# Kernel optimization log

Hardware: AMD Instinct MI355X
Metric: run time of the kernel (lower is better)

The kernel has to match this reference:

```python
import jax, jax.numpy as jnp
import numpy as np
import math

D_MODEL = 512
EXPAND = 2
D_INNER = EXPAND * D_MODEL          # 1024
HEADDIM = 16
NHEADS = D_INNER // HEADDIM         # 64
NGROUPS = 1
D_STATE = 16
D_CONV = 4
CHUNK = 256
CONV_DIM = D_INNER + 2 * NGROUPS * D_STATE      # 1056
D_IN_PROJ = 2 * D_INNER + 2 * NGROUPS * D_STATE + NHEADS  # 2144
EPS = 1e-5


def setup_inputs() -> dict:
    key = jax.random.key(0)
    ks = jax.random.split(key, 9)
    B, L = 2, 4096
    u = jax.random.normal(ks[0], (B, L, D_MODEL), dtype=jnp.float32)
    in_proj_w = jax.random.normal(ks[1], (D_IN_PROJ, D_MODEL), dtype=jnp.float32) * (1.0 / math.sqrt(D_MODEL))
    conv_w = jax.random.normal(ks[2], (CONV_DIM, D_CONV), dtype=jnp.float32) * (1.0 / math.sqrt(D_CONV))
    conv_b = jnp.zeros((CONV_DIM,), dtype=jnp.float32)
    # dt_bias = inverse-softplus of dt sampled log-uniform in [1e-3, 1e-1]
    dt = jnp.exp(jax.random.uniform(ks[3], (NHEADS,)) * (math.log(0.1) - math.log(0.001)) + math.log(0.001))
    dt_bias = dt + jnp.log(-jnp.expm1(-dt))
    A_log = jnp.log(jax.random.uniform(ks[4], (NHEADS,), minval=1.0, maxval=16.0))
    D_skip = jnp.ones((NHEADS,), dtype=jnp.float32)
    norm_w = jnp.ones((D_INNER,), dtype=jnp.float32)
    out_proj_w = jax.random.normal(ks[5], (D_MODEL, D_INNER), dtype=jnp.float32) * (1.0 / math.sqrt(D_INNER))
    return {"u": u, "in_proj_w": in_proj_w, "conv_w": conv_w, "conv_b": conv_b,
            "dt_bias": dt_bias, "A_log": A_log, "D_skip": D_skip,
            "norm_w": norm_w, "out_proj_w": out_proj_w}


def _segsum(x):
    # x: (..., T) -> (..., T, T) lower-triangular cumulative segment sums
    T = x.shape[-1]
    cs = jnp.cumsum(x, axis=-1)
    s = cs[..., :, None] - cs[..., None, :]
    mask = jnp.tril(jnp.ones((T, T), dtype=bool))
    return jnp.where(mask, s, -jnp.inf)


def _ssd(xdt, dA, Bm, Cm):
    # xdt: (b,l,h,p) already multiplied by dt; dA: (b,l,h); Bm,Cm: (b,l,h,n)
    b, l, h, p = xdt.shape
    n = Bm.shape[-1]
    nc = l // CHUNK
    xr = xdt.reshape(b, nc, CHUNK, h, p)
    Br = Bm.reshape(b, nc, CHUNK, h, n)
    Cr = Cm.reshape(b, nc, CHUNK, h, n)
    dAr = dA.reshape(b, nc, CHUNK, h).transpose(0, 3, 1, 2)  # (b,h,nc,c)
    A_cs = jnp.cumsum(dAr, axis=-1)
    # intra-chunk (diagonal blocks)
    Ldec = jnp.exp(_segsum(dAr))                              # (b,h,nc,c,c)
    Y_diag = jnp.einsum('bclhn,bcshn,bhcls,bcshp->bclhp', Cr, Br, Ldec, xr)
    # per-chunk final states
    decay_states = jnp.exp(A_cs[..., -1:] - A_cs)             # (b,h,nc,c)
    states = jnp.einsum('bclhn,bhcl,bclhp->bchpn', Br, decay_states, xr)
    states = jnp.concatenate([jnp.zeros_like(states[:, :1]), states], axis=1)
    chunk_sums = jnp.pad(A_cs[..., -1], ((0, 0), (0, 0), (1, 0)))  # (b,h,nc+1)
    decay_chunk = jnp.exp(_segsum(chunk_sums))                # (b,h,nc+1,nc+1)
    new_states = jnp.einsum('bhzc,bchpn->bzhpn', decay_chunk, states)
    prev_states = new_states[:, :-1]                          # (b,nc,h,p,n)
    # inter-chunk contribution
    state_decay_out = jnp.exp(A_cs)                           # (b,h,nc,c)
    Y_off = jnp.einsum('bclhn,bchpn,bhcl->bclhp', Cr, prev_states, state_decay_out)
    return (Y_diag + Y_off).reshape(b, l, h, p)


def _forward(u, in_proj_w, conv_w, conv_b, dt_bias, A_log, D_skip, norm_w, out_proj_w):
    b, l, _ = u.shape
    zxbcdt = jnp.einsum('bld,ed->ble', u, in_proj_w)
    z = zxbcdt[..., :D_INNER]
    xBC = zxbcdt[..., D_INNER:D_INNER + CONV_DIM]
    dt = zxbcdt[..., D_INNER + CONV_DIM:]
    dt = jax.nn.softplus(dt + dt_bias)                        # (b,l,h)
    # causal depthwise conv1d + silu
    xBC_t = xBC.transpose(0, 2, 1)                            # (b, conv_dim, l)
    conv_out = jax.lax.conv_general_dilated(
        xBC_t, conv_w[:, None, :], window_strides=(1,),
        padding=[(D_CONV - 1, 0)], feature_group_count=CONV_DIM,
        dimension_numbers=('NCH', 'OIH', 'NCH'))
    xBC = jax.nn.silu((conv_out + conv_b[None, :, None]).transpose(0, 2, 1))
    x = xBC[..., :D_INNER].reshape(b, l, NHEADS, HEADDIM)
    Bg = xBC[..., D_INNER:D_INNER + NGROUPS * D_STATE].reshape(b, l, NGROUPS, D_STATE)
    Cg = xBC[..., D_INNER + NGROUPS * D_STATE:].reshape(b, l, NGROUPS, D_STATE)
    hpg = NHEADS // NGROUPS
    Bm = jnp.repeat(Bg, hpg, axis=2)                          # (b,l,h,n)
    Cm = jnp.repeat(Cg, hpg, axis=2)
    A = -jnp.exp(A_log)                                       # (h,)
    dA = dt * A                                               # (b,l,h)
    y = _ssd(x * dt[..., None], dA, Bm, Cm)
    y = y + x * D_skip[None, None, :, None]
    y = y.reshape(b, l, D_INNER)
    # gated RMSNorm (norm_before_gate=False): norm(y * silu(z)) * w
    y = y * jax.nn.silu(z)
    y = y * jax.lax.rsqrt(jnp.mean(y * y, axis=-1, keepdims=True) + EPS) * norm_w
    return jnp.einsum('ble,de->bld', y, out_proj_w)


def reference(u, in_proj_w, conv_w, conv_b, dt_bias, A_log, D_skip, norm_w, out_proj_w):
    return _forward(u, in_proj_w, conv_w, conv_b, dt_bias, A_log, D_skip, norm_w, out_proj_w)
```

## Files before the change

kernel.cpp:

```cpp
#include <hip/hip_runtime.h>
#include <hip/hip_bf16.h>
#include <math.h>

#define D_MODEL   512
#define D_INNER   1024
#define NHEADS    64
#define HEADDIM   16
#define D_STATE   16
#define CONV_DIM  1056
#define D_IN_PROJ 2144
#define CHUNK     256
#define NCHUNK    16
#define BATCH     2
#define SEQ       4096
#define ROWS      (BATCH * SEQ)
#define LDZX      2176

typedef __bf16    bf16x8 __attribute__((ext_vector_type(8)));
typedef _Float16  f16x8  __attribute__((ext_vector_type(8)));
typedef float     f32x4  __attribute__((ext_vector_type(4)));
typedef float     f32x16 __attribute__((ext_vector_type(16)));
typedef unsigned short u16x8 __attribute__((ext_vector_type(8)));
typedef unsigned int   u32x4 __attribute__((ext_vector_type(4)));

__device__ __forceinline__ float softplusf(float x) {
    return (x > 20.f) ? x : log1pf(expf(x));
}
__device__ __forceinline__ float siluf(float x) {
    return x / (1.f + expf(-x));
}
__device__ __forceinline__ unsigned short f2b(float x) {
    union { __hip_bfloat16 h; unsigned short u; } cv;
    cv.h = __float2bfloat16(x);
    return cv.u;
}
__device__ __forceinline__ float b2f(unsigned short u) {
    union { float f; unsigned int i; } c;
    c.i = (unsigned int)u << 16;
    return c.f;
}
__device__ __forceinline__ void load_lds16(const unsigned short* g, unsigned short* l) {
    __builtin_amdgcn_global_load_lds(
        (const __attribute__((address_space(1))) void*)g,
        (__attribute__((address_space(3))) void*)l,
        16, 0, 0);
}

__global__ __launch_bounds__(256) void cast8(const float* __restrict__ in,
                                             unsigned short* __restrict__ out, int n) {
    int i = (blockIdx.x * blockDim.x + threadIdx.x) * 8;
    if (i >= n) return;
    float4 a = *(const float4*)(in + i);
    float4 b = *(const float4*)(in + i + 4);
    u16x8 o;
    o[0] = f2b(a.x); o[1] = f2b(a.y); o[2] = f2b(a.z); o[3] = f2b(a.w);
    o[4] = f2b(b.x); o[5] = f2b(b.y); o[6] = f2b(b.z); o[7] = f2b(b.w);
    *(u16x8*)(out + i) = o;
}

__global__ __launch_bounds__(256) void castpad8(const float* __restrict__ in,
                                                unsigned short* __restrict__ out,
                                                int n, int npad) {
    int i = (blockIdx.x * blockDim.x + threadIdx.x) * 8;
    if (i >= npad) return;
    u16x8 o;
    if (i + 8 <= n) {
        float4 a = *(const float4*)(in + i);
        float4 b = *(const float4*)(in + i + 4);
        o[0] = f2b(a.x); o[1] = f2b(a.y); o[2] = f2b(a.z); o[3] = f2b(a.w);
        o[4] = f2b(b.x); o[5] = f2b(b.y); o[6] = f2b(b.z); o[7] = f2b(b.w);
    } else {
        #pragma unroll
        for (int j = 0; j < 8; ++j) o[j] = (i + j < n) ? f2b(in[i + j]) : (unsigned short)0;
    }
    *(u16x8*)(out + i) = o;
}

__global__ __launch_bounds__(256) void gemm_mfma(const unsigned short* __restrict__ A,
                                                 const unsigned short* __restrict__ B,
                                                 float* __restrict__ C32,
                                                 unsigned short* __restrict__ C16,
                                                 float* __restrict__ dtout,
                                                 int Nout, int K, int lda, int ldc16) {
    __shared__ unsigned short As[2][128 * 32];
    __shared__ unsigned short Bs[2][128 * 32];
    const int t    = threadIdx.x;
    const int wave = t >> 6;
    const int lane = t & 63;
    const int bm   = blockIdx.y * 128;
    const int bn   = blockIdx.x * 128;
    const int wr   = wave >> 1;
    const int wc   = wave & 1;

    const int srow = wave * 16 + (lane >> 2);
    const int scol = (lane & 3) * 8;
    const unsigned short* ga0 = A + (size_t)(bm + srow) * lda + scol;
    const unsigned short* ga1 = A + (size_t)(bm + 64 + srow) * lda + scol;
    const unsigned short* gb0 = B + (size_t)(bn + srow) * K + scol;
    const unsigned short* gb1 = B + (size_t)(bn + 64 + srow) * K + scol;

    const int fr = lane & 15;
    const int kb = (lane >> 4) * 8;

    f32x4 acc[4][4] = {};
    const int NIT = K >> 5;

    load_lds16(ga0, &As[0][wave * 512]);
    load_lds16(ga1, &As[0][2048 + wave * 512]);
    load_lds16(gb0, &Bs[0][wave * 512]);
    load_lds16(gb1, &Bs[0][2048 + wave * 512]);
    __syncthreads();

    int cur = 0;
    for (int it = 0; it < NIT; ++it) {
        if (it + 1 < NIT) {
            const int k0 = (it + 1) * 32;
            const int nb = cur ^ 1;
            load_lds16(ga0 + k0, &As[nb][wave * 512]);
            load_lds16(ga1 + k0, &As[nb][2048 + wave * 512]);
            load_lds16(gb0 + k0, &Bs[nb][wave * 512]);
            load_lds16(gb1 + k0, &Bs[nb][2048 + wave * 512]);
        }
        const unsigned short* Ab = As[cur];
        const unsigned short* Bb = Bs[cur];
        bf16x8 af[4], bfr[4];
        #pragma unroll
        for (int m = 0; m < 4; ++m)
            af[m] = *reinterpret_cast<const bf16x8*>(&Ab[(wr * 64 + m * 16 + fr) * 32 + kb]);
        #pragma unroll
        for (int n = 0; n < 4; ++n)
            bfr[n] = *reinterpret_cast<const bf16x8*>(&Bb[(wc * 64 + n * 16 + fr) * 32 + kb]);
        #pragma unroll
        for (int m = 0; m < 4; ++m)
            #pragma unroll
            for (int n = 0; n < 4; ++n)
                acc[m][n] = __builtin_amdgcn_mfma_f32_16x16x32_bf16(af[m], bfr[n], acc[m][n], 0, 0, 0);
        __syncthreads();
        cur ^= 1;
    }

    const int cr0 = bm + wr * 64 + ((lane >> 4) << 2);
    const int cc0 = bn + wc * 64 + (lane & 15);
    if (C16) {
        #pragma unroll
        for (int m = 0; m < 4; ++m) {
            #pragma unroll
            for (int n = 0; n < 4; ++n) {
                const int col = cc0 + n * 16;
                #pragma unroll
                for (int j = 0; j < 4; ++j) {
                    const int row = cr0 + m * 16 + j;
                    float v = acc[m][n][j];
                    C16[(size_t)row * ldc16 + col] = f2b(v);
                    if (dtout && col >= 2080 && col < 2144)
                        dtout[(size_t)row * 64 + (col - 2080)] = v;
                }
            }
        }
    } else {
        #pragma unroll
        for (int m = 0; m < 4; ++m) {
            #pragma unroll
            for (int n = 0; n < 4; ++n) {
                const int col = cc0 + n * 16;
                if (col < Nout) {
                    #pragma unroll
                    for (int j = 0; j < 4; ++j)
                        C32[(size_t)(cr0 + m * 16 + j) * Nout + col] = acc[m][n][j];
                }
            }
        }
    }
}

__global__ void conv_silu4(const unsigned short* __restrict__ zxb, const float* __restrict__ cw,
                           const float* __restrict__ cb, unsigned short* __restrict__ xcb) {
    int idx = blockIdx.x * blockDim.x + threadIdx.x;
    if (idx >= ROWS * (CONV_DIM / 4)) return;
    int cq = idx % (CONV_DIM / 4);
    int bl = idx / (CONV_DIM / 4);
    int l  = bl % SEQ;
    int c4 = cq * 4;
    const unsigned short* base = zxb + (size_t)bl * LDZX + D_INNER + c4;
    float4 w0 = *(const float4*)(cw + (c4 + 0) * 4);
    float4 w1 = *(const float4*)(cw + (c4 + 1) * 4);
    float4 w2 = *(const float4*)(cw + (c4 + 2) * 4);
    float4 w3 = *(const float4*)(cw + (c4 + 3) * 4);
    float4 zf = make_float4(0.f, 0.f, 0.f, 0.f);
    float4 x3 = zf, x2 = zf, x1 = zf, x0;
    ushort4 u0 = *(const ushort4*)(base);
    x0 = make_float4(b2f(u0.x), b2f(u0.y), b2f(u0.z), b2f(u0.w));
    if (l >= 1) { ushort4 u1 = *(const ushort4*)(base - 1 * LDZX);
                  x1 = make_float4(b2f(u1.x), b2f(u1.y), b2f(u1.z), b2f(u1.w)); }
    if (l >= 2) { ushort4 u2 = *(const ushort4*)(base - 2 * LDZX);
                  x2 = make_float4(b2f(u2.x), b2f(u2.y), b2f(u2.z), b2f(u2.w)); }
    if (l >= 3) { ushort4 u3 = *(const ushort4*)(base - 3 * LDZX);
                  x3 = make_float4(b2f(u3.x), b2f(u3.y), b2f(u3.z), b2f(u3.w)); }
    float4 bb = *(const float4*)(cb + c4);
    ushort4 r;
    r.x = f2b(siluf(bb.x + w0.x * x3.x + w0.y * x2.x + w0.z * x1.x + w0.w * x0.x));
    r.y = f2b(siluf(bb.y + w1.x * x3.y + w1.y * x2.y + w1.z * x1.y + w1.w * x0.y));
    r.z = f2b(siluf(bb.z + w2.x * x3.z + w2.y * x2.z + w2.z * x1.z + w2.w * x0.z));
    r.w = f2b(siluf(bb.w + w3.x * x3.w + w3.y * x2.w + w3.z * x1.w + w3.w * x0.w));
    *(ushort4*)(xcb + (size_t)bl * CONV_DIM + c4) = r;
}

__global__ void dt_softplus(const float* __restrict__ dt_raw, const float* __restrict__ dtb,
                            float* __restrict__ dtsp) {
    int idx = blockIdx.x * blockDim.x + threadIdx.x;
    if (idx >= ROWS * NHEADS) return;
    int h = idx & 63;
    dtsp[idx] = softplusf(dt_raw[idx] + dtb[h]);
}

__global__ __launch_bounds__(256, 3) void ssd_chunk(const unsigned short* __restrict__ xcb,
                                                    const float* __restrict__ dtsp,
                                                    const float* __restrict__ A_log,
                                                    float* __restrict__ ypre,
                                                    float* __restrict__ states,
                                                    float* __restrict__ csb,
                                                    float* __restrict__ csum) {
    __shared__ _Float16 Bb[256][16];
    __shared__ _Float16 Cb[256][16];
    __shared__ _Float16 Xt[16][264];
    __shared__ _Float16 Xdt[16][264];
    __shared__ _Float16 Bt[16][264];
    __shared__ float csL[256];
    __shared__ float wsumL[4];
    __shared__ float stpart[4][16][16];

    const int bid = blockIdx.x;
    const int h = bid & 63;
    const int c = (bid >> 6) & 15;
    const int b = bid >> 10;
    const int t = threadIdx.x;
    const int wv = t >> 6;
    const int lane = t & 63;
    const int fr = lane & 15;
    const int hi = lane >> 4;
    const int l31 = lane & 31;
    const int hi5 = lane >> 5;
    const int row = b * SEQ + c * CHUNK + t;

    float Ah  = -__expf(A_log[h]);
    float dtv = dtsp[(size_t)row * NHEADS + h];
    float val = dtv * Ah;
    #pragma unroll
    for (int off = 1; off < 64; off <<= 1) {
        float o = __shfl_up(val, off, 64);
        if (lane >= off) val += o;
    }
    if (lane == 63) wsumL[wv] = val;
    __syncthreads();
    float pre = 0.f, cl = 0.f;
    #pragma unroll
    for (int w2 = 0; w2 < 4; ++w2) {
        float s = wsumL[w2];
        if (w2 < wv) pre += s;
        cl += s;
    }
    float cst = val + pre;
    csL[t] = cst;
    csb[(size_t)bid * 256 + t] = cst;
    if (t == 0) csum[(b * 64 + h) * 16 + c] = cl;
    float dec_t = __expf(cl - cst);

    const unsigned short* xrow = xcb + (size_t)row * CONV_DIM;
    u16x8 braw0 = *(const u16x8*)(xrow + D_INNER);
    u16x8 braw1 = *(const u16x8*)(xrow + D_INNER + 8);
    u16x8 craw0 = *(const u16x8*)(xrow + D_INNER + D_STATE);
    u16x8 craw1 = *(const u16x8*)(xrow + D_INNER + D_STATE + 8);
    u16x8 xraw0 = *(const u16x8*)(xrow + h * HEADDIM);
    u16x8 xraw1 = *(const u16x8*)(xrow + h * HEADDIM + 8);
    float bv[16], cv[16], xv[16];
    #pragma unroll
    for (int n = 0; n < 8; ++n) {
        bv[n] = b2f(braw0[n]); bv[8 + n] = b2f(braw1[n]);
        cv[n] = b2f(craw0[n]); cv[8 + n] = b2f(craw1[n]);
        xv[n] = b2f(xraw0[n]); xv[8 + n] = b2f(xraw1[n]);
    }
    {
        f16x8 pk;
        #pragma unroll
        for (int n = 0; n < 8; ++n) pk[n] = (_Float16)cv[n];
        *(f16x8*)&Cb[t][0] = pk;
        #pragma unroll
        for (int n = 0; n < 8; ++n) pk[n] = (_Float16)cv[8 + n];
        *(f16x8*)&Cb[t][8] = pk;
        #pragma unroll
        for (int n = 0; n < 8; ++n) pk[n] = (_Float16)bv[n];
        *(f16x8*)&Bb[t][0] = pk;
        #pragma unroll
        for (int n = 0; n < 8; ++n) pk[n] = (_Float16)bv[8 + n];
        *(f16x8*)&Bb[t][8] = pk;
    }
    #pragma unroll
    for (int n = 0; n < 16; ++n) {
        Bt[n][t] = (_Float16)bv[n];
        float xd = xv[n] * dtv;
        Xt[n][t] = (_Float16)xd;
        Xdt[n][t] = (_Float16)(xd * dec_t);
    }
    __syncthreads();

    const int browbase = b * SEQ + c * CHUNK;
    const f32x16 z16 = {};

    #pragma unroll
    for (int halfi = 0; halfi < 2; ++halfi) {
        const int rt = (halfi == 0) ? wv : 7 - wv;
        const int t0 = rt * 32;
        const float cs_t = csL[t0 + l31];
        const f16x8 cfrag = *(const f16x8*)&Cb[t0 + l31][hi5 * 8];
        f32x16 yacc = {};
        for (int sb = 0; sb <= rt; ++sb) {
            const int s0 = sb * 32;
            f16x8 bfrag = *(const f16x8*)&Bb[s0 + l31][hi5 * 8];
            f32x16 sp = __builtin_amdgcn_mfma_f32_32x32x16_f16(bfrag, cfrag, z16, 0, 0, 0);
            const bool diag = (sb == rt);
            unsigned int D[8];
            #pragma unroll
            for (int j = 0; j < 8; ++j) {
                const int q0 = 2 * j;
                const int sr0 = (q0 & 3) + 8 * (q0 >> 2) + 4 * hi5;
                float p0 = sp[q0] * __expf(cs_t - csL[s0 + sr0]);
                float p1 = sp[q0 + 1] * __expf(cs_t - csL[s0 + sr0 + 1]);
                if (diag) {
                    p0 = (sr0 <= l31) ? p0 : 0.f;
                    p1 = (sr0 + 1 <= l31) ? p1 : 0.f;
                }
                D[j] = __builtin_bit_cast(unsigned int, __builtin_amdgcn_cvt_pkrtz(p0, p1));
            }
            unsigned int pD[8];
            #pragma unroll
            for (int j = 0; j < 8; ++j) pD[j] = (unsigned int)__shfl_xor((int)D[j], 32, 64);
            u32x4 fa;
            fa[0] = hi5 ? pD[2] : D[0];
            fa[1] = hi5 ? pD[3] : D[1];
            fa[2] = hi5 ? D[2] : pD[0];
            fa[3] = hi5 ? D[3] : pD[1];
            f16x8 pf0 = __builtin_bit_cast(f16x8, fa);
            f16x8 xf0 = *(const f16x8*)&Xt[fr][s0 + hi5 * 8];
            yacc = __builtin_amdgcn_mfma_f32_32x32x16_f16(pf0, xf0, yacc, 0, 0, 0);
            fa[0] = hi5 ? pD[6] : D[4];
            fa[1] = hi5 ? pD[7] : D[5];
            fa[2] = hi5 ? D[6] : pD[4];
            fa[3] = hi5 ? D[7] : pD[5];
            f16x8 pf1 = __builtin_bit_cast(f16x8, fa);
            f16x8 xf1 = *(const f16x8*)&Xt[fr][s0 + 16 + hi5 * 8];
            yacc = __builtin_amdgcn_mfma_f32_32x32x16_f16(pf1, xf1, yacc, 0, 0, 0);
        }
        if (l31 < 16) {
            #pragma unroll
            for (int q = 0; q < 16; ++q) {
                const int tr = t0 + (q & 3) + 8 * (q >> 2) + 4 * hi5;
                ypre[(size_t)(browbase + tr) * D_INNER + h * HEADDIM + l31] = yacc[q];
            }
        }
    }

    const int r0w = wv * 64;
    f32x4 stacc = {};
    #pragma unroll
    for (int kt = 0; kt < 2; ++kt) {
        f16x8 xa = *(const f16x8*)&Xdt[fr][r0w + kt * 32 + hi * 8];
        f16x8 bb2 = *(const f16x8*)&Bt[fr][r0w + kt * 32 + hi * 8];
        stacc = __builtin_amdgcn_mfma_f32_16x16x32_f16(xa, bb2, stacc, 0, 0, 0);
    }
    #pragma unroll
    for (int j = 0; j < 4; ++j)
        stpart[wv][hi * 4 + j][fr] = stacc[j];
    __syncthreads();
    {
        const int p = t >> 4, n = t & 15;
        float st = stpart[0][p][n] + stpart[1][p][n] + stpart[2][p][n] + stpart[3][p][n];
        states[(size_t)bid * 256 + t] = st;
    }
}

__global__ __launch_bounds__(256) void ssd_rec(const float* __restrict__ states,
                                               const float* __restrict__ csum,
                                               float* __restrict__ prevst) {
    const int bh = blockIdx.x;
    const int b = bh >> 6, h = bh & 63;
    const int t = threadIdx.x;
    float run = 0.f;
    for (int c = 0; c < NCHUNK; ++c) {
        size_t idx = ((size_t)((b * 16 + c) * 64 + h)) * 256 + t;
        prevst[idx] = run;
        run = run * expf(csum[bh * 16 + c]) + states[idx];
    }
}

__global__ __launch_bounds__(512, 4) void ssd_off_norm(const unsigned short* __restrict__ xcb,
                                                       const unsigned short* __restrict__ zxb,
                                                       const float* __restrict__ ypre,
                                                       const float* __restrict__ prevst,
                                                       const float* __restrict__ csb,
                                                       const float* __restrict__ Dskip,
                                                       const float* __restrict__ normw,
                                                       unsigned short* __restrict__ yout) {
    __shared__ float Cs[16][16];
    __shared__ float csS[64][16];
    __shared__ float nw[1024];
    __shared__ float Dn[64];
    __shared__ float red[16][8];

    const int blk = blockIdx.x;
    const int bc = blk >> 4;
    const int rb = blk & 15;
    const int r0 = rb * 16;
    const int b = bc >> 4, c = bc & 15;
    const int brow0 = b * SEQ + c * CHUNK;
    const int t = threadIdx.x;
    const int ch0 = t * 2;
    const int h = ch0 >> 4;
    const int p0 = ch0 & 15;
    const int wv = t >> 6;
    const int lane = t & 63;

    if (t < 256) *(float4*)&nw[t * 4] = *(const float4*)(normw + t * 4);
    else if (t < 320) Dn[t - 256] = Dskip[t - 256];
    if (t < 64) {
        int r = t >> 2, n4 = (t & 3) * 4;
        ushort4 uu = *(const ushort4*)(xcb + (size_t)(brow0 + r0 + r) * CONV_DIM
                                       + D_INNER + D_STATE + n4);
        Cs[r][n4 + 0] = b2f(uu.x); Cs[r][n4 + 1] = b2f(uu.y);
        Cs[r][n4 + 2] = b2f(uu.z); Cs[r][n4 + 3] = b2f(uu.w);
    }
    #pragma unroll
    for (int i = t; i < 1024; i += 512) {
        int r = i & 15, hh = i >> 4;
        csS[hh][r] = csb[(size_t)(bc * 64 + hh) * 256 + r0 + r];
    }

    float ps[2][16];
    {
        const float* pbase = prevst + (size_t)(bc * 64 + h) * 256 + p0 * 16;
        #pragma unroll
        for (int n4 = 0; n4 < 16; n4 += 4) {
            *(float4*)&ps[0][n4] = *(const float4*)(pbase + n4);
            *(float4*)&ps[1][n4] = *(const float4*)(pbase + 16 + n4);
        }
    }
    __syncthreads();

    const float d = Dn[h];
    const float nw0 = nw[ch0], nw1 = nw[ch0 + 1];

    for (int r = 0; r < 16; ++r) {
        const size_t grow = (size_t)(brow0 + r0 + r);
        float2 yv = *(const float2*)(ypre + grow * D_INNER + ch0);
        ushort2 xu = *(const ushort2*)(xcb + grow * CONV_DIM + ch0);
        ushort2 zu = *(const ushort2*)(zxb + grow * LDZX + ch0);
        float sdo = __expf(csS[h][r]);
        float off0 = 0.f, off1 = 0.f;
        #pragma unroll
        for (int n = 0; n < 16; ++n) {
            float cn = Cs[r][n];
            off0 += cn * ps[0][n];
            off1 += cn * ps[1][n];
        }
        float g0 = (yv.x + sdo * off0 + b2f(xu.x) * d) * siluf(b2f(zu.x));
        float g1 = (yv.y + sdo * off1 + b2f(xu.y) * d) * siluf(b2f(zu.y));
        float s = g0 * g0 + g1 * g1;
        #pragma unroll
        for (int o = 32; o > 0; o >>= 1) s += __shfl_down(s, o, 64);
        if (lane == 0) red[r][wv] = s;
        __syncthreads();
        float tot = 0.f;
        #pragma unroll
        for (int w2 = 0; w2 < 8; ++w2) tot += red[r][w2];
        float rstd = rsqrtf(tot * (1.f / (float)D_INNER) + 1e-5f);
        ushort2 o2;
        o2.x = f2b(g0 * rstd * nw0);
        o2.y = f2b(g1 * rstd * nw1);
        *(ushort2*)(yout + grow * D_INNER + ch0) = o2;
    }
}

extern "C" void kernel_launch(void* const* d_in, const int* in_sizes, int n_in,
                              void* d_out, int out_size, void* d_ws, size_t ws_size,
                              hipStream_t stream) {
    const float* u     = (const float*)d_in[0];
    const float* Win   = (const float*)d_in[1];
    const float* cw    = (const float*)d_in[2];
    const float* cb    = (const float*)d_in[3];
    const float* dtb   = (const float*)d_in[4];
    const float* Alog  = (const float*)d_in[5];
    const float* Dsk   = (const float*)d_in[6];
    const float* normw = (const float*)d_in[7];
    const float* Wout  = (const float*)d_in[8];
    float* out = (float*)d_out;

    float* ws = (float*)d_ws;
    unsigned short* zxb = (unsigned short*)ws;
    float* dt_raw = ws + 8912896;
    float* dtsp   = dt_raw + 524288;
    float* csb    = dtsp + 524288;
    float* st     = csb + 524288;
    float* pst    = st + 524288;
    float* csum   = pst + 524288;
    float* ypre   = csum + 2048;
    unsigned short* xcb   = (unsigned short*)(ypre + 8388608);
    unsigned short* yn_bf = (unsigned short*)((float*)xcb + 4325376);
    unsigned short* u_bf  = (unsigned short*)((float*)yn_bf + 2097152);
    unsigned short* win_bf  = (unsigned short*)((float*)u_bf + 2097152);
    unsigned short* wout_bf = (unsigned short*)((float*)win_bf + 557056);

    cast8<<<2048, 256, 0, stream>>>(u, u_bf, 4194304);
    castpad8<<<544, 256, 0, stream>>>(Win, win_bf, 2144 * 512, 2176 * 512);
    cast8<<<256, 256, 0, stream>>>(Wout, wout_bf, 524288);

    gemm_mfma<<<dim3(17, 64), 256, 0, stream>>>(u_bf, win_bf, nullptr, zxb, dt_raw,
                                                D_IN_PROJ, D_MODEL, D_MODEL, LDZX);

    conv_silu4<<<(ROWS * (CONV_DIM / 4)) / 256, 256, 0, stream>>>(zxb, cw, cb, xcb);
    dt_softplus<<<(ROWS * NHEADS) / 256, 256, 0, stream>>>(dt_raw, dtb, dtsp);
    ssd_chunk<<<BATCH * NCHUNK * NHEADS, 256, 0, stream>>>(xcb, dtsp, Alog, ypre, st, csb, csum);
    ssd_rec<<<BATCH * NHEADS, 256, 0, stream>>>(st, csum, pst);
    ssd_off_norm<<<512, 512, 0, stream>>>(xcb, zxb, ypre, pst, csb, Dsk, normw, yn_bf);

    gemm_mfma<<<dim3(4, 64), 256, 0, stream>>>(yn_bf, wout_bf, out, nullptr, nullptr,
                                               D_MODEL, D_INNER, D_INNER, 0);
}
```

Before: 156.4 us.

## Fuse dt softplus into GEMM, store ypre in bf16, swizzle grid, tile conv

The in-projection GEMM now applies softplus plus bias to the dt columns in its epilogue, which removes the separate dt_softplus kernel and its extra buffer. The bf16 output is staged through LDS so global stores are coalesced 16-byte writes, and a 1D swizzled block order is meant to improve L2 reuse. The intra-chunk SSD output ypre is stored as bf16 instead of fp32, halving that traffic at some cost in precision. The conv kernel computes four rows per thread to reuse overlapping input loads, and ssd_rec preloads states and decays into registers and shared memory.

```diff
diff --git a/kernel.cpp b/kernel.cpp
--- a/kernel.cpp
+++ b/kernel.cpp
@@ -80,17 +80,22 @@
                                                  const unsigned short* __restrict__ B,
                                                  float* __restrict__ C32,
                                                  unsigned short* __restrict__ C16,
-                                                 float* __restrict__ dtout,
-                                                 int Nout, int K, int lda, int ldc16) {
-    __shared__ unsigned short As[2][128 * 32];
-    __shared__ unsigned short Bs[2][128 * 32];
+                                                 float* __restrict__ dtsp,
+                                                 const float* __restrict__ dtb,
+                                                 int K, int lda, int ldc16, int nbx) {
+    __shared__ unsigned short smem[16384];
     const int t    = threadIdx.x;
     const int wave = t >> 6;
     const int lane = t & 63;
-    const int bm   = blockIdx.y * 128;
-    const int bn   = blockIdx.x * 128;
-    const int wr   = wave >> 1;
-    const int wc   = wave & 1;
+    const int cpx = gridDim.x >> 3;
+    const int bid = blockIdx.x;
+    const int swz = (bid & 7) * cpx + (bid >> 3);
+    const int by = swz / nbx;
+    const int bx = swz - by * nbx;
+    const int bm = by * 128;
+    const int bn = bx * 128;
+    const int wr = wave >> 1;
+    const int wc = wave & 1;
 
     const int srow = wave * 16 + (lane >> 2);
     const int scol = (lane & 3) * 8;
@@ -105,10 +110,10 @@
     f32x4 acc[4][4] = {};
     const int NIT = K >> 5;
 
-    load_lds16(ga0, &As[0][wave * 512]);
-    load_lds16(ga1, &As[0][2048 + wave * 512]);
-    load_lds16(gb0, &Bs[0][wave * 512]);
-    load_lds16(gb1, &Bs[0][2048 + wave * 512]);
+    load_lds16(ga0, smem + wave * 512);
+    load_lds16(ga1, smem + 2048 + wave * 512);
+    load_lds16(gb0, smem + 8192 + wave * 512);
+    load_lds16(gb1, smem + 8192 + 2048 + wave * 512);
     __syncthreads();
 
     int cur = 0;
@@ -116,13 +121,13 @@
         if (it + 1 < NIT) {
             const int k0 = (it + 1) * 32;
             const int nb = cur ^ 1;
-            load_lds16(ga0 + k0, &As[nb][wave * 512]);
-            load_lds16(ga1 + k0, &As[nb][2048 + wave * 512]);
-            load_lds16(gb0 + k0, &Bs[nb][wave * 512]);
-            load_lds16(gb1 + k0, &Bs[nb][2048 + wave * 512]);
-        }
-        const unsigned short* Ab = As[cur];
-        const unsigned short* Bb = Bs[cur];
+            load_lds16(ga0 + k0, smem + nb * 4096 + wave * 512);
+            load_lds16(ga1 + k0, smem + nb * 4096 + 2048 + wave * 512);
+            load_lds16(gb0 + k0, smem + 8192 + nb * 4096 + wave * 512);
+            load_lds16(gb1 + k0, smem + 8192 + nb * 4096 + 2048 + wave * 512);
+        }
+        const unsigned short* Ab = smem + cur * 4096;
+        const unsigned short* Bb = smem + 8192 + cur * 4096;
         bf16x8 af[4], bfr[4];
         #pragma unroll
         for (int m = 0; m < 4; ++m)
@@ -139,84 +144,99 @@
         cur ^= 1;
     }
 
-    const int cr0 = bm + wr * 64 + ((lane >> 4) << 2);
-    const int cc0 = bn + wc * 64 + (lane & 15);
     if (C16) {
+        if (dtsp && bn == 2048) {
+            #pragma unroll
+            for (int m = 0; m < 4; ++m) {
+                #pragma unroll
+                for (int n = 0; n < 4; ++n) {
+                    const int col = bn + wc * 64 + fr + n * 16;
+                    if (col >= 2080 && col < 2144) {
+                        const int h = col - 2080;
+                        const float bias = dtb[h];
+                        #pragma unroll
+                        for (int j = 0; j < 4; ++j) {
+                            const int row = bm + wr * 64 + ((lane >> 4) << 2) + m * 16 + j;
+                            dtsp[(size_t)row * 64 + h] = softplusf(acc[m][n][j] + bias);
+                        }
+                    }
+                }
+            }
+        }
         #pragma unroll
         for (int m = 0; m < 4; ++m) {
             #pragma unroll
             for (int n = 0; n < 4; ++n) {
-                const int col = cc0 + n * 16;
+                const int lcol = wc * 64 + fr + n * 16;
                 #pragma unroll
                 for (int j = 0; j < 4; ++j) {
-                    const int row = cr0 + m * 16 + j;
-                    float v = acc[m][n][j];
-                    C16[(size_t)row * ldc16 + col] = f2b(v);
-                    if (dtout && col >= 2080 && col < 2144)
-                        dtout[(size_t)row * 64 + (col - 2080)] = v;
+                    const int lrow = wr * 64 + ((lane >> 4) << 2) + m * 16 + j;
+                    smem[lrow * 128 + lcol] = f2b(acc[m][n][j]);
                 }
             }
         }
+        __syncthreads();
+        #pragma unroll
+        for (int p = 0; p < 8; ++p) {
+            const int r = p * 16 + (t >> 4);
+            const int cl = (t & 15) * 8;
+            u16x8 v = *(const u16x8*)&smem[r * 128 + cl];
+            *(u16x8*)(C16 + (size_t)(bm + r) * ldc16 + bn + cl) = v;
+        }
     } else {
-        #pragma unroll
-        for (int m = 0; m < 4; ++m) {
-            #pragma unroll
-            for (int n = 0; n < 4; ++n) {
-                const int col = cc0 + n * 16;
-                if (col < Nout) {
-                    #pragma unroll
-                    for (int j = 0; j < 4; ++j)
-                        C32[(size_t)(cr0 + m * 16 + j) * Nout + col] = acc[m][n][j];
-                }
-            }
-        }
-    }
-}
-
-__global__ void conv_silu4(const unsigned short* __restrict__ zxb, const float* __restrict__ cw,
-                           const float* __restrict__ cb, unsigned short* __restrict__ xcb) {
+        const int cr0 = bm + wr * 64 + ((lane >> 4) << 2);
+        const int cc0 = bn + wc * 64 + fr;
+        #pragma unroll
+        for (int m = 0; m < 4; ++m)
+            #pragma unroll
+            for (int n = 0; n < 4; ++n)
+                #pragma unroll
+                for (int j = 0; j < 4; ++j)
+                    C32[(size_t)(cr0 + m * 16 + j) * 512 + cc0 + n * 16] = acc[m][n][j];
+    }
+}
+
+__global__ void conv_silu44(const unsigned short* __restrict__ zxb, const float* __restrict__ cw,
+                            const float* __restrict__ cb, unsigned short* __restrict__ xcb) {
     int idx = blockIdx.x * blockDim.x + threadIdx.x;
-    if (idx >= ROWS * (CONV_DIM / 4)) return;
-    int cq = idx % (CONV_DIM / 4);
-    int bl = idx / (CONV_DIM / 4);
-    int l  = bl % SEQ;
-    int c4 = cq * 4;
-    const unsigned short* base = zxb + (size_t)bl * LDZX + D_INNER + c4;
+    if (idx >= (ROWS / 4) * (CONV_DIM / 4)) return;
+    const int cq  = idx % (CONV_DIM / 4);
+    const int blq = idx / (CONV_DIM / 4);
+    const int bl0 = blq * 4;
+    const int l0  = bl0 % SEQ;
+    const int c4  = cq * 4;
+    const unsigned short* base = zxb + (size_t)bl0 * LDZX + D_INNER + c4;
     float4 w0 = *(const float4*)(cw + (c4 + 0) * 4);
     float4 w1 = *(const float4*)(cw + (c4 + 1) * 4);
     float4 w2 = *(const float4*)(cw + (c4 + 2) * 4);
     float4 w3 = *(const float4*)(cw + (c4 + 3) * 4);
-    float4 zf = make_float4(0.f, 0.f, 0.f, 0.f);
-    float4 x3 = zf, x2 = zf, x1 = zf, x0;
-    ushort4 u0 = *(const ushort4*)(base);
-    x0 = make_float4(b2f(u0.x), b2f(u0.y), b2f(u0.z), b2f(u0.w));
-    if (l >= 1) { ushort4 u1 = *(const ushort4*)(base - 1 * LDZX);
-                  x1 = make_float4(b2f(u1.x), b2f(u1.y), b2f(u1.z), b2f(u1.w)); }
-    if (l >= 2) { ushort4 u2 = *(const ushort4*)(base - 2 * LDZX);
-                  x2 = make_float4(b2f(u2.x), b2f(u2.y), b2f(u2.z), b2f(u2.w)); }
-    if (l >= 3) { ushort4 u3 = *(const ushort4*)(base - 3 * LDZX);
-                  x3 = make_float4(b2f(u3.x), b2f(u3.y), b2f(u3.z), b2f(u3.w)); }
     float4 bb = *(const float4*)(cb + c4);
-    ushort4 r;
-    r.x = f2b(siluf(bb.x + w0.x * x3.x + w0.y * x2.x + w0.z * x1.x + w0.w * x0.x));
-    r.y = f2b(siluf(bb.y + w1.x * x3.y + w1.y * x2.y + w1.z * x1.y + w1.w * x0.y));
-    r.z = f2b(siluf(bb.z + w2.x * x3.z + w2.y * x2.z + w2.z * x1.z + w2.w * x0.z));
-    r.w = f2b(siluf(bb.w + w3.x * x3.w + w3.y * x2.w + w3.z * x1.w + w3.w * x0.w));
-    *(ushort4*)(xcb + (size_t)bl * CONV_DIM + c4) = r;
-}
-
-__global__ void dt_softplus(const float* __restrict__ dt_raw, const float* __restrict__ dtb,
-                            float* __restrict__ dtsp) {
-    int idx = blockIdx.x * blockDim.x + threadIdx.x;
-    if (idx >= ROWS * NHEADS) return;
-    int h = idx & 63;
-    dtsp[idx] = softplusf(dt_raw[idx] + dtb[h]);
+    float4 in[7];
+    #pragma unroll
+    for (int k = 0; k < 7; ++k) {
+        const int off = k - 3;
+        if (l0 == 0 && k < 3) {
+            in[k] = make_float4(0.f, 0.f, 0.f, 0.f);
+        } else {
+            ushort4 uu = *(const ushort4*)(base + (long)off * LDZX);
+            in[k] = make_float4(b2f(uu.x), b2f(uu.y), b2f(uu.z), b2f(uu.w));
+        }
+    }
+    #pragma unroll
+    for (int r = 0; r < 4; ++r) {
+        ushort4 o;
+        o.x = f2b(siluf(bb.x + w0.x * in[r].x + w0.y * in[r + 1].x + w0.z * in[r + 2].x + w0.w * in[r + 3].x));
+        o.y = f2b(siluf(bb.y + w1.x * in[r].y + w1.y * in[r + 1].y + w1.z * in[r + 2].y + w1.w * in[r + 3].y));
+        o.z = f2b(siluf(bb.z + w2.x * in[r].z + w2.y * in[r + 1].z + w2.z * in[r + 2].z + w2.w * in[r + 3].z));
+        o.w = f2b(siluf(bb.w + w3.x * in[r].w + w3.y * in[r + 1].w + w3.z * in[r + 2].w + w3.w * in[r + 3].w));
+        *(ushort4*)(xcb + (size_t)(bl0 + r) * CONV_DIM + c4) = o;
+    }
 }
 
 __global__ __launch_bounds__(256, 3) void ssd_chunk(const unsigned short* __restrict__ xcb,
                                                     const float* __restrict__ dtsp,
                                                     const float* __restrict__ A_log,
-                                                    float* __restrict__ ypre,
+                                                    unsigned short* __restrict__ ypre16,
                                                     float* __restrict__ states,
                                                     float* __restrict__ csb,
                                                     float* __restrict__ csum) {
@@ -354,7 +374,7 @@
             #pragma unroll
             for (int q = 0; q < 16; ++q) {
                 const int tr = t0 + (q & 3) + 8 * (q >> 2) + 4 * hi5;
-                ypre[(size_t)(browbase + tr) * D_INNER + h * HEADDIM + l31] = yacc[q];
+                ypre16[(size_t)(browbase + tr) * D_INNER + h * HEADDIM + l31] = f2b(yacc[q]);
             }
         }
     }
@@ -381,20 +401,27 @@
 __global__ __launch_bounds__(256) void ssd_rec(const float* __restrict__ states,
                                                const float* __restrict__ csum,
                                                float* __restrict__ prevst) {
+    __shared__ float dec[16];
     const int bh = blockIdx.x;
     const int b = bh >> 6, h = bh & 63;
     const int t = threadIdx.x;
+    if (t < 16) dec[t] = __expf(csum[bh * 16 + t]);
+    float sv[16];
+    #pragma unroll
+    for (int c = 0; c < NCHUNK; ++c)
+        sv[c] = states[((size_t)((b * 16 + c) * 64 + h)) * 256 + t];
+    __syncthreads();
     float run = 0.f;
+    #pragma unroll
     for (int c = 0; c < NCHUNK; ++c) {
-        size_t idx = ((size_t)((b * 16 + c) * 64 + h)) * 256 + t;
-        prevst[idx] = run;
-        run = run * expf(csum[bh * 16 + c]) + states[idx];
+        prevst[((size_t)((b * 16 + c) * 64 + h)) * 256 + t] = run;
+        run = run * dec[c] + sv[c];
     }
 }
 
 __global__ __launch_bounds__(512, 4) void ssd_off_norm(const unsigned short* __restrict__ xcb,
                                                        const unsigned short* __restrict__ zxb,
-                                                       const float* __restrict__ ypre,
+                                                       const unsigned short* __restrict__ ypre16,
                                                        const float* __restrict__ prevst,
                                                        const float* __restrict__ csb,
                                                        const float* __restrict__ Dskip,
@@ -450,7 +477,7 @@
 
     for (int r = 0; r < 16; ++r) {
         const size_t grow = (size_t)(brow0 + r0 + r);
-        float2 yv = *(const float2*)(ypre + grow * D_INNER + ch0);
+        ushort2 yu = *(const ushort2*)(ypre16 + grow * D_INNER + ch0);
         ushort2 xu = *(const ushort2*)(xcb + grow * CONV_DIM + ch0);
         ushort2 zu = *(const ushort2*)(zxb + grow * LDZX + ch0);
         float sdo = __expf(csS[h][r]);
@@ -461,8 +488,8 @@
             off0 += cn * ps[0][n];
             off1 += cn * ps[1][n];
         }
-        float g0 = (yv.x + sdo * off0 + b2f(xu.x) * d) * siluf(b2f(zu.x));
-        float g1 = (yv.y + sdo * off1 + b2f(xu.y) * d) * siluf(b2f(zu.y));
+        float g0 = (b2f(yu.x) + sdo * off0 + b2f(xu.x) * d) * siluf(b2f(zu.x));
+        float g1 = (b2f(yu.y) + sdo * off1 + b2f(xu.y) * d) * siluf(b2f(zu.y));
         float s = g0 * g0 + g1 * g1;
         #pragma unroll
         for (int o = 32; o > 0; o >>= 1) s += __shfl_down(s, o, 64);
@@ -495,16 +522,15 @@
 
     float* ws = (float*)d_ws;
     unsigned short* zxb = (unsigned short*)ws;
-    float* dt_raw = ws + 8912896;
-    float* dtsp   = dt_raw + 524288;
+    float* dtsp   = ws + 8912896;
     float* csb    = dtsp + 524288;
     float* st     = csb + 524288;
     float* pst    = st + 524288;
     float* csum   = pst + 524288;
-    float* ypre   = csum + 2048;
-    unsigned short* xcb   = (unsigned short*)(ypre + 8388608);
-    unsigned short* yn_bf = (unsigned short*)((float*)xcb + 4325376);
-    unsigned short* u_bf  = (unsigned short*)((float*)yn_bf + 2097152);
+    unsigned short* ypre16 = (unsigned short*)(csum + 2048);
+    unsigned short* xcb    = (unsigned short*)((float*)ypre16 + 4194304);
+    unsigned short* yn_bf  = (unsigned short*)((float*)xcb + 4325376);
+    unsigned short* u_bf   = (unsigned short*)((float*)yn_bf + 2097152);
     unsigned short* win_bf  = (unsigned short*)((float*)u_bf + 2097152);
     unsigned short* wout_bf = (unsigned short*)((float*)win_bf + 557056);
 
@@ -512,15 +538,14 @@
     castpad8<<<544, 256, 0, stream>>>(Win, win_bf, 2144 * 512, 2176 * 512);
     cast8<<<256, 256, 0, stream>>>(Wout, wout_bf, 524288);
 
-    gemm_mfma<<<dim3(17, 64), 256, 0, stream>>>(u_bf, win_bf, nullptr, zxb, dt_raw,
-                                                D_IN_PROJ, D_MODEL, D_MODEL, LDZX);
-
-    conv_silu4<<<(ROWS * (CONV_DIM / 4)) / 256, 256, 0, stream>>>(zxb, cw, cb, xcb);
-    dt_softplus<<<(ROWS * NHEADS) / 256, 256, 0, stream>>>(dt_raw, dtb, dtsp);
-    ssd_chunk<<<BATCH * NCHUNK * NHEADS, 256, 0, stream>>>(xcb, dtsp, Alog, ypre, st, csb, csum);
+    gemm_mfma<<<1088, 256, 0, stream>>>(u_bf, win_bf, nullptr, zxb, dtsp, dtb,
+                                        D_MODEL, D_MODEL, LDZX, 17);
+
+    conv_silu44<<<(ROWS / 4) * (CONV_DIM / 4) / 256, 256, 0, stream>>>(zxb, cw, cb, xcb);
+    ssd_chunk<<<BATCH * NCHUNK * NHEADS, 256, 0, stream>>>(xcb, dtsp, Alog, ypre16, st, csb, csum);
     ssd_rec<<<BATCH * NHEADS, 256, 0, stream>>>(st, csum, pst);
-    ssd_off_norm<<<512, 512, 0, stream>>>(xcb, zxb, ypre, pst, csb, Dsk, normw, yn_bf);
-
-    gemm_mfma<<<dim3(4, 64), 256, 0, stream>>>(yn_bf, wout_bf, out, nullptr, nullptr,
-                                               D_MODEL, D_INNER, D_INNER, 0);
-}
+    ssd_off_norm<<<512, 512, 0, stream>>>(xcb, zxb, ypre16, pst, csb, Dsk, normw, yn_bf);
+
+    gemm_mfma<<<256, 256, 0, stream>>>(yn_bf, wout_bf, out, nullptr, nullptr, nullptr,
+                                       D_INNER, D_INNER, 0, 4);
+}
```

Result: faster. 149.5 us (-4.4%).
